# Optimization experiments

Measured on AMD Instinct MI355X. Metric: run time of the kernel, lower is better.

Reference implementation:

```python
import jax, jax.numpy as jnp
import numpy as np

WS = 8          # window size
NH = 4          # num heads
DIM = 64
HID = 256       # mlp_ratio * dim
EPS = 1e-5


def _rel_pos_index(ws):
    coords = np.stack(np.meshgrid(np.arange(ws), np.arange(ws), indexing='ij')).reshape(2, -1)
    rel = (coords[:, :, None] - coords[:, None, :]).transpose(1, 2, 0)  # (N,N,2)
    rel[..., 0] += ws - 1
    rel[..., 1] += ws - 1
    rel[..., 0] *= 2 * ws - 1
    return rel.sum(-1)  # (N,N)


def _layernorm(x, g, b):
    mu = x.mean(-1, keepdims=True)
    var = ((x - mu) ** 2).mean(-1, keepdims=True)
    return (x - mu) * jax.lax.rsqrt(var + EPS) * g + b


def setup_inputs() -> dict:
    key = jax.random.key(0)
    ks = jax.random.split(key, 16)
    s = 0.02
    return {
        'x': jax.random.normal(ks[0], (8, DIM, 256, 256), jnp.float32),
        'qkv_w': jax.random.normal(ks[1], (DIM, 3 * DIM), jnp.float32) * s,
        'qkv_b': jnp.zeros((3 * DIM,), jnp.float32),
        'proj_w': jax.random.normal(ks[2], (DIM, DIM), jnp.float32) * s,
        'proj_b': jnp.zeros((DIM,), jnp.float32),
        'rpb_table': jax.random.normal(ks[3], ((2 * WS - 1) ** 2, NH), jnp.float32) * s,
        'norm1_g': jnp.ones((DIM,), jnp.float32),
        'norm1_b': jnp.zeros((DIM,), jnp.float32),
        'norm2_g': jnp.ones((DIM,), jnp.float32),
        'norm2_b': jnp.zeros((DIM,), jnp.float32),
        'ffn_w1': jax.random.normal(ks[4], (DIM, HID), jnp.float32) * s,
        'ffn_b1': jnp.zeros((HID,), jnp.float32),
        'ffn_w2': jax.random.normal(ks[5], (HID, DIM), jnp.float32) * s,
        'ffn_w2_b': jnp.zeros((DIM,), jnp.float32),
        'dw_w': jax.random.normal(ks[6], (DIM, 1, 3, 3), jnp.float32) * s,
        'dw_b': jnp.zeros((DIM,), jnp.float32),
    }


def reference(x, qkv_w, qkv_b, proj_w, proj_b, rpb_table,
              norm1_g, norm1_b, norm2_g, norm2_b,
              ffn_w1, ffn_b1, ffn_w2, ffn_w2_b, dw_w, dw_b):
    B, C, H, W = x.shape
    ws, nh = WS, NH
    hd = C // nh
    N = ws * ws
    assert H % ws == 0 and W % ws == 0  # chosen shapes avoid reflect pad

    x_hw = jnp.transpose(x, (0, 2, 3, 1))  # (B,H,W,C)

    # --- window attention branch ---
    xn = _layernorm(x_hw, norm1_g, norm1_b)
    win = xn.reshape(B, H // ws, ws, W // ws, ws, C).transpose(0, 1, 3, 2, 4, 5)
    win = win.reshape(-1, N, C)  # (B*nW, N, C)

    qkv = win @ qkv_w + qkv_b  # (BnW, N, 3C)
    qkv = qkv.reshape(-1, N, 3, nh, hd).transpose(2, 0, 3, 1, 4)
    q, k, v = qkv[0], qkv[1], qkv[2]  # (BnW, nh, N, hd)

    scale = hd ** -0.5
    attn = jnp.einsum('bhnd,bhmd->bhnm', q, k) * scale
    idx = _rel_pos_index(ws)
    bias = rpb_table[idx.reshape(-1)].reshape(N, N, nh).transpose(2, 0, 1)  # (nh,N,N)
    attn = jax.nn.softmax(attn + bias[None], axis=-1)
    out = jnp.einsum('bhnm,bhmd->bhnd', attn, v)
    out = out.transpose(0, 2, 1, 3).reshape(-1, N, C)
    out = out @ proj_w + proj_b

    out = out.reshape(B, H // ws, W // ws, ws, ws, C).transpose(0, 1, 3, 2, 4, 5)
    out = out.reshape(B, H, W, C)
    x_hw = x_hw + out

    # --- FFN + depthwise conv branch ---
    xn = _layernorm(x_hw, norm2_g, norm2_b)
    ffn = jax.nn.gelu(xn @ ffn_w1 + ffn_b1, approximate=False) @ ffn_w2 + ffn_w2_b

    xc = jnp.transpose(x_hw, (0, 3, 1, 2))  # (B,C,H,W)
    xc = jax.lax.conv_general_dilated(
        xc, dw_w, window_strides=(1, 1), padding=((1, 1), (1, 1)),
        feature_group_count=C,
        dimension_numbers=('NCHW', 'OIHW', 'NCHW')) + dw_b[None, :, None, None]
    xc = jnp.transpose(xc, (0, 2, 3, 1))

    x_hw = x_hw + ffn + xc
    return jnp.transpose(x_hw, (0, 3, 1, 2))  # (B,C,H,W)
```

## Files before the change

kernel.cpp:

```cpp
#include <hip/hip_runtime.h>
#include <cmath>


typedef __attribute__((ext_vector_type(8))) short bf16x8;
typedef __attribute__((ext_vector_type(4))) short s16x4;
typedef __attribute__((ext_vector_type(4))) float f32x4;
typedef __attribute__((ext_vector_type(2))) __bf16 bfv2;
typedef __attribute__((ext_vector_type(4))) __bf16 bfv4;

static __device__ __forceinline__ unsigned short f2bf(float f) {
  return __builtin_bit_cast(unsigned short, (__bf16)f);
}
static __device__ __forceinline__ unsigned f2bf2(float a, float b) {
  bfv2 v; v.x = (__bf16)a; v.y = (__bf16)b;
  return __builtin_bit_cast(unsigned, v);
}
static __device__ __forceinline__ s16x4 f2bf4(f32x4 f) {
  bfv4 v; v.x = (__bf16)f[0]; v.y = (__bf16)f[1]; v.z = (__bf16)f[2]; v.w = (__bf16)f[3];
  return __builtin_bit_cast(s16x4, v);
}
static __device__ __forceinline__ float bf2f(unsigned short u) {
  union { unsigned u; float f; } v; v.u = ((unsigned)u) << 16;
  return v.f;
}
static __device__ __forceinline__ float bf2f_s(short s) { return bf2f((unsigned short)s); }

static __device__ __forceinline__ int swz(int row, int c) {
  return row * 72 + ((((c >> 3) ^ (row >> 3)) & 7) << 3) + (c & 7);
}
static __device__ __forceinline__ int swzg(int row, int g) {
  return row * 72 + (((g ^ (row >> 3)) & 7) << 3);
}

#define MFMA32(a, b, c) __builtin_amdgcn_mfma_f32_16x16x32_bf16(a, b, c, 0, 0, 0)

#if __has_builtin(__builtin_amdgcn_mfma_f32_16x16x16bf16_1k)
static __device__ __forceinline__ f32x4 MFMA16(s16x4 a, s16x4 b, f32x4 c) {
  return __builtin_amdgcn_mfma_f32_16x16x16bf16_1k(a, b, c, 0, 0, 0);
}
#else
static __device__ __forceinline__ f32x4 MFMA16(s16x4 a, s16x4 b, f32x4 c) {
  bf16x8 a8 = (bf16x8){a[0], a[1], a[2], a[3], 0, 0, 0, 0};
  bf16x8 b8 = (bf16x8){b[0], b[1], b[2], b[3], 0, 0, 0, 0};
  return __builtin_amdgcn_mfma_f32_16x16x32_bf16(a8, b8, c, 0, 0, 0);
}
#endif

__global__ void pack_weights_kernel(const float* __restrict__ qkv_w,
                                    const float* __restrict__ proj_w,
                                    const float* __restrict__ w1,
                                    const float* __restrict__ w2,
                                    const float* __restrict__ rpb,
                                    unsigned short* __restrict__ qkvt,
                                    unsigned short* __restrict__ projt,
                                    unsigned short* __restrict__ w1t,
                                    unsigned short* __restrict__ w2t,
                                    float* __restrict__ biasg) {
  const int t = blockIdx.x * 256 + threadIdx.x;
  {
    const int n = t >> 6, k = t & 63;
    if (n < 192) {
      float v = qkv_w[k * 192 + n];
      if (n < 64) v *= 0.25f;
      qkvt[t] = f2bf(v);
    }
    if (n < 64)  projt[t] = f2bf(proj_w[k * 64 + n]);
    w1t[t] = f2bf(w1[k * 256 + n]);
  }
  {
    const int n = t >> 8, k = t & 255;
    w2t[t] = f2bf(w2[k * 64 + n]);
  }
  {
    const int i = (t >> 6) & 63, j = t & 63, h = t >> 12;
    const int ridx = ((i >> 3) - (j >> 3) + 7) * 15 + ((i & 7) - (j & 7) + 7);
    biasg[t] = rpb[ridx * 4 + h];
  }
}

__global__ __launch_bounds__(512, 2)
void win_attn_kernel(const float* __restrict__ x,
                     const unsigned short* __restrict__ qkvt,
                     const float* __restrict__ qkv_b,
                     const unsigned short* __restrict__ projt,
                     const float* __restrict__ proj_b,
                     const float* __restrict__ biasg,
                     const float* __restrict__ n1g,
                     const float* __restrict__ n1b,
                     unsigned short* __restrict__ x1b)
{
  __shared__ unsigned short xw[2 * 4608];
  __shared__ unsigned short xn[2 * 4608];

  const int tid = threadIdx.x;
  const int bid = blockIdx.x;
  const int wid = ((bid & 7) << 9) | (bid >> 3);
  const int b   = wid >> 9;
  const int wy  = (wid >> 4) & 31;
  const int wxp = wid & 15;
  const int y0 = wy << 3, x0 = wxp << 4;

  const size_t imgbase = (size_t)b << 22;
#pragma unroll
  for (int i = 0; i < 16; ++i) {
    const int idx = i * 512 + tid;
    const int c = idx >> 7, t = idx & 127;
    const int ty = t >> 4, tx = t & 15;
    const float v = x[imgbase + ((size_t)c << 16) + (size_t)(y0 + ty) * 256 + (x0 + tx)];
    const int wn = tx >> 3, tok = (ty << 3) | (tx & 7);
    xw[wn * 4608 + swz(tok, c)] = f2bf(v);
  }
  __syncthreads();

  {
    const int t2 = tid >> 2, q = tid & 3;
    const int wn = t2 >> 6, tok = t2 & 63;
    const unsigned short* xwp = xw + wn * 4608;
    const bf16x8 h0 = *(const bf16x8*)&xwp[swzg(tok, 2 * q)];
    const bf16x8 h1 = *(const bf16x8*)&xwp[swzg(tok, 2 * q + 1)];
    float xv[16], s = 0.f, s2 = 0.f;
#pragma unroll
    for (int j = 0; j < 8; ++j) { xv[j] = bf2f_s(h0[j]); xv[8 + j] = bf2f_s(h1[j]); }
#pragma unroll
    for (int j = 0; j < 16; ++j) { s += xv[j]; s2 += xv[j] * xv[j]; }
    s  += __shfl_xor(s, 1);  s  += __shfl_xor(s, 2);
    s2 += __shfl_xor(s2, 1); s2 += __shfl_xor(s2, 2);
    const float mu   = s * 0.015625f;
    const float rstd = rsqrtf(s2 * 0.015625f - mu * mu + 1e-5f);
#pragma unroll
    for (int j = 0; j < 8; ++j) {
      const int c = q * 16 + j * 2;
      const float a0 = (xv[j * 2 + 0] - mu) * rstd * n1g[c]     + n1b[c];
      const float a1 = (xv[j * 2 + 1] - mu) * rstd * n1g[c + 1] + n1b[c + 1];
      *(unsigned*)&xn[wn * 4608 + swz(tok, c)] = f2bf2(a0, a1);
    }
  }
  __syncthreads();

  const int lane = tid & 63;
  const int w8   = tid >> 6;
  const int wn   = w8 >> 2;
  const int g    = w8 & 3;
  const int lr   = lane & 15;
  const int lg   = lane >> 4;
  const unsigned short* xnp = xn + wn * 4608;
  const unsigned short* xwp = xw + wn * 4608;
  unsigned short*       xnw = xn + wn * 4608;

  bf16x8 afr[4][2];
#pragma unroll
  for (int mt = 0; mt < 4; ++mt)
#pragma unroll
    for (int ks = 0; ks < 2; ++ks)
      afr[mt][ks] = *(const bf16x8*)&xnp[swzg(mt * 16 + lr, ks * 4 + lg)];
  __syncthreads();

  const int nbq = g * 16, nbk = 64 + g * 16, nbv = 128 + g * 16;
  f32x4 dqT[4], dkT[4], dv[4];
  {
    const float4 qb = *(const float4*)&qkv_b[nbq + lg * 4];
    const float4 kb = *(const float4*)&qkv_b[nbk + lg * 4];
    const float  vb = qkv_b[nbv + lr];
    const f32x4 qbv = (f32x4){qb.x * 0.25f, qb.y * 0.25f, qb.z * 0.25f, qb.w * 0.25f};
    const f32x4 kbv = (f32x4){kb.x, kb.y, kb.z, kb.w};
    const f32x4 vbv = (f32x4){vb, vb, vb, vb};
#pragma unroll
    for (int u = 0; u < 4; ++u) { dqT[u] = qbv; dkT[u] = kbv; dv[u] = vbv; }
  }
#pragma unroll
  for (int ks = 0; ks < 2; ++ks) {
    const bf16x8 wq = *(const bf16x8*)&qkvt[(nbq + lr) * 64 + ks * 32 + lg * 8];
    const bf16x8 wk = *(const bf16x8*)&qkvt[(nbk + lr) * 64 + ks * 32 + lg * 8];
    const bf16x8 wv = *(const bf16x8*)&qkvt[(nbv + lr) * 64 + ks * 32 + lg * 8];
#pragma unroll
    for (int u = 0; u < 4; ++u) {
      dqT[u] = MFMA32(wq, afr[u][ks], dqT[u]);
      dkT[u] = MFMA32(wk, afr[u][ks], dkT[u]);
      dv[u]  = MFMA32(afr[u][ks], wv, dv[u]);
    }
  }
  s16x4 qf[4], kf[4], vf[4];
#pragma unroll
  for (int u = 0; u < 4; ++u) { qf[u] = f2bf4(dqT[u]); kf[u] = f2bf4(dkT[u]); vf[u] = f2bf4(dv[u]); }

  f32x4 sacc[4][4];
#pragma unroll
  for (int mt = 0; mt < 4; ++mt)
#pragma unroll
    for (int nt = 0; nt < 4; ++nt) {
      const float4 bb = *(const float4*)&biasg[(g << 12) + (nt * 16 + lr) * 64 + mt * 16 + lg * 4];
      sacc[mt][nt] = MFMA16(kf[mt], qf[nt], (f32x4){bb.x, bb.y, bb.z, bb.w});
    }

  s16x4 pa[4][4];
#pragma unroll
  for (int nt = 0; nt < 4; ++nt) {
    float sum = 0.f;
#pragma unroll
    for (int mt = 0; mt < 4; ++mt)
#pragma unroll
      for (int r = 0; r < 4; ++r) { const float e = __expf(sacc[mt][nt][r]); sacc[mt][nt][r] = e; sum += e; }
    sum += __shfl_xor(sum, 16);
    sum += __shfl_xor(sum, 32);
    const float rs = 1.f / sum;
#pragma unroll
    for (int mt = 0; mt < 4; ++mt)
      pa[mt][nt] = f2bf4(sacc[mt][nt] * rs);
  }

  f32x4 o[4];
#pragma unroll
  for (int nt = 0; nt < 4; ++nt) {
    o[nt] = (f32x4){0,0,0,0};
#pragma unroll
    for (int mt = 0; mt < 4; ++mt)
      o[nt] = MFMA16(pa[mt][nt], vf[mt], o[nt]);
  }
#pragma unroll
  for (int nt = 0; nt < 4; ++nt)
#pragma unroll
    for (int r = 0; r < 4; ++r)
      xnw[swz(nt * 16 + lg * 4 + r, g * 16 + lr)] = f2bf(o[nt][r]);
  __syncthreads();

  {
    bf16x8 pa2[4][2];
#pragma unroll
    for (int mt = 0; mt < 4; ++mt)
#pragma unroll
      for (int ks = 0; ks < 2; ++ks)
        pa2[mt][ks] = *(const bf16x8*)&xnp[swzg(mt * 16 + lr, ks * 4 + lg)];
    __syncthreads();

    const float pbias = proj_b[g * 16 + lr];
    f32x4 d2[4];
#pragma unroll
    for (int mt = 0; mt < 4; ++mt) d2[mt] = (f32x4){pbias, pbias, pbias, pbias};
#pragma unroll
    for (int ks = 0; ks < 2; ++ks) {
      const bf16x8 pb = *(const bf16x8*)&projt[(g * 16 + lr) * 64 + ks * 32 + lg * 8];
#pragma unroll
      for (int mt = 0; mt < 4; ++mt)
        d2[mt] = MFMA32(pa2[mt][ks], pb, d2[mt]);
    }
#pragma unroll
    for (int mt = 0; mt < 4; ++mt)
#pragma unroll
      for (int r = 0; r < 4; ++r) {
        const int tok = mt * 16 + lg * 4 + r;
        const float val = d2[mt][r] + bf2f(xwp[swz(tok, g * 16 + lr)]);
        xnw[swz(tok, g * 16 + lr)] = f2bf(val);
      }
  }
  __syncthreads();

#pragma unroll
  for (int i = 0; i < 2; ++i) {
    const int u = i * 512 + tid;
    const int tk = u >> 3, gr = u & 7;
    const int wn2 = tk >> 6, tok = tk & 63;
    const bf16x8 v = *(const bf16x8*)&xn[wn2 * 4608 + swzg(tok, gr)];
    *(bf16x8*)&x1b[(((size_t)b * 256 + y0 + (tok >> 3)) * 256 + x0 + wn2 * 8 + (tok & 7)) * 64 + gr * 8] = v;
  }
}

__global__ __launch_bounds__(256, 2)
void ffn_conv_kernel(const unsigned short* __restrict__ x1b,
                     const float* __restrict__ n2g, const float* __restrict__ n2b,
                     const unsigned short* __restrict__ w1t, const float* __restrict__ b1,
                     const unsigned short* __restrict__ w2t, const float* __restrict__ b2,
                     const float* __restrict__ dww, const float* __restrict__ dwb,
                     float* __restrict__ out)
{
  __shared__ __align__(16) unsigned short pool[20000];
  unsigned short* x1h = pool;
  unsigned short* xnb = pool + 7200;
  unsigned short* hid = pool + 11808;
  float*          d2f = (float*)(pool + 7200);

  const int tid = threadIdx.x;
  const int bid = blockIdx.x;
  const int wid = ((bid & 7) << 10) | (bid >> 3);
  const int b  = wid >> 10;
  const int wy = (wid >> 5) & 31;
  const int wx = wid & 31;
  const int y0 = wy << 3, x0 = wx << 3;

  const int lane = tid & 63;
  const int g    = tid >> 6;
  const int lr   = lane & 15;
  const int lg   = lane >> 4;

#pragma unroll
  for (int i = 0; i < 7; ++i) {
    const int u = i * 256 + tid;
    if (u < 1600) {
      const int p = u >> 4, c4 = (u & 15) << 2;
      const int py = p / 10, px = p - py * 10;
      const int gy = y0 + py - 1, gx = x0 + px - 1;
      uint2 v = make_uint2(0u, 0u);
      if ((unsigned)gy < 256u && (unsigned)gx < 256u)
        v = *(const uint2*)&x1b[(((size_t)b * 256 + gy) * 256 + gx) * 64 + c4];
      *(uint2*)&x1h[p * 72 + c4] = v;
    }
  }
  __syncthreads();

  {
    const int t = tid >> 2, q = tid & 3;
    const int pp = ((t >> 3) + 1) * 10 + (t & 7) + 1;
    const bf16x8 h0 = *(const bf16x8*)&x1h[pp * 72 + q * 16];
    const bf16x8 h1 = *(const bf16x8*)&x1h[pp * 72 + q * 16 + 8];
    float xv[16], s = 0.f, s2 = 0.f;
#pragma unroll
    for (int j = 0; j < 8; ++j) { xv[j] = bf2f_s(h0[j]); xv[8 + j] = bf2f_s(h1[j]); }
#pragma unroll
    for (int j = 0; j < 16; ++j) { s += xv[j]; s2 += xv[j] * xv[j]; }
    s  += __shfl_xor(s, 1);  s  += __shfl_xor(s, 2);
    s2 += __shfl_xor(s2, 1); s2 += __shfl_xor(s2, 2);
    const float mu   = s * 0.015625f;
    const float rstd = rsqrtf(s2 * 0.015625f - mu * mu + 1e-5f);
#pragma unroll
    for (int j = 0; j < 8; ++j) {
      const int c = q * 16 + j * 2;
      const float a0 = (xv[j * 2 + 0] - mu) * rstd * n2g[c]     + n2b[c];
      const float a1 = (xv[j * 2 + 1] - mu) * rstd * n2g[c + 1] + n2b[c + 1];
      *(unsigned*)&xnb[swz(t, c)] = f2bf2(a0, a1);
    }
  }
  __syncthreads();

  bf16x8 afr[4][2];
#pragma unroll
  for (int mt = 0; mt < 4; ++mt)
#pragma unroll
    for (int ks = 0; ks < 2; ++ks)
      afr[mt][ks] = *(const bf16x8*)&xnb[swzg(mt * 16 + lr, ks * 4 + lg)];

  const float b2n = b2[g * 16 + lr];
  f32x4 d2[4];
#pragma unroll
  for (int mt = 0; mt < 4; ++mt) d2[mt] = (f32x4){b2n, b2n, b2n, b2n};

#pragma unroll
  for (int half = 0; half < 2; ++half) {
#pragma unroll
    for (int nt = 0; nt < 2; ++nt) {
      const int nb = half * 128 + g * 32 + nt * 16;
      const float4 bb = *(const float4*)&b1[nb + lg * 4];
      f32x4 d1[4];
#pragma unroll
      for (int mt = 0; mt < 4; ++mt) d1[mt] = (f32x4){bb.x, bb.y, bb.z, bb.w};
#pragma unroll
      for (int ks = 0; ks < 2; ++ks) {
        const bf16x8 aw = *(const bf16x8*)&w1t[(nb + lr) * 64 + ks * 32 + lg * 8];
#pragma unroll
        for (int mt = 0; mt < 4; ++mt)
          d1[mt] = MFMA32(aw, afr[mt][ks], d1[mt]);
      }
#pragma unroll
      for (int mt = 0; mt < 4; ++mt) {
        f32x4 hv;
#pragma unroll
        for (int r = 0; r < 4; ++r) {
          const float e = __expf(-1.702f * d1[mt][r]);
          hv[r] = __fdividef(d1[mt][r], 1.f + e);
        }
        const s16x4 pk = f2bf4(hv);
        const int row  = mt * 16 + lr;
        const int nl   = g * 32 + nt * 16 + lg * 4;
        const int addr = row * 128 + (((nl >> 3) ^ (row & 7)) << 3) + (nl & 7);
        *(s16x4*)&hid[addr] = pk;
      }
    }
    __syncthreads();

#pragma unroll
    for (int ks2 = 0; ks2 < 4; ++ks2) {
      const bf16x8 bw = *(const bf16x8*)&w2t[(g * 16 + lr) * 256 + half * 128 + ks2 * 32 + lg * 8];
#pragma unroll
      for (int mt = 0; mt < 4; ++mt) {
        const int row  = mt * 16 + lr;
        const int gran = ks2 * 4 + lg;
        const bf16x8 ah = *(const bf16x8*)&hid[row * 128 + ((gran ^ (row & 7)) << 3)];
        d2[mt] = MFMA32(ah, bw, d2[mt]);
      }
    }
    __syncthreads();
  }

  {
#pragma unroll
    for (int mt = 0; mt < 4; ++mt)
#pragma unroll
      for (int r = 0; r < 4; ++r)
        d2f[(mt * 16 + lg * 4 + r) * 65 + g * 16 + lr] = d2[mt][r];
  }
  __syncthreads();

  {
    const int cty = lane >> 3, ctx = lane & 7;
    float cacc[16];
#pragma unroll
    for (int i = 0; i < 16; ++i) cacc[i] = dwb[g * 16 + i];
#pragma unroll
    for (int dy = 0; dy < 3; ++dy)
#pragma unroll
      for (int dx = 0; dx < 3; ++dx) {
        const int p = (cty + dy) * 10 + (ctx + dx);
        const bf16x8 h0 = *(const bf16x8*)&x1h[p * 72 + g * 16];
        const bf16x8 h1 = *(const bf16x8*)&x1h[p * 72 + g * 16 + 8];
        const bool ctr = (dy == 1) && (dx == 1);
#pragma unroll
        for (int i = 0; i < 8; ++i) {
          float w0  = dww[(g * 16 + i) * 9     + dy * 3 + dx];
          float w1_ = dww[(g * 16 + 8 + i) * 9 + dy * 3 + dx];
          if (ctr) { w0 += 1.f; w1_ += 1.f; }
          cacc[i]     += w0  * bf2f_s(h0[i]);
          cacc[8 + i] += w1_ * bf2f_s(h1[i]);
        }
      }
    const size_t obase = ((size_t)b * 64 + g * 16) * 65536 + (size_t)(y0 + cty) * 256 + (x0 + ctx);
#pragma unroll
    for (int i = 0; i < 16; ++i)
      out[obase + (size_t)i * 65536] = cacc[i] + d2f[lane * 65 + g * 16 + i];
  }
}

extern "C" void kernel_launch(void* const* d_in, const int* in_sizes, int n_in,
                              void* d_out, int out_size, void* d_ws, size_t ws_size,
                              hipStream_t stream) {
  const float* x      = (const float*)d_in[0];
  const float* qkv_w  = (const float*)d_in[1];
  const float* qkv_b  = (const float*)d_in[2];
  const float* proj_w = (const float*)d_in[3];
  const float* proj_b = (const float*)d_in[4];
  const float* rpb    = (const float*)d_in[5];
  const float* n1g    = (const float*)d_in[6];
  const float* n1b    = (const float*)d_in[7];
  const float* n2g    = (const float*)d_in[8];
  const float* n2b    = (const float*)d_in[9];
  const float* w1     = (const float*)d_in[10];
  const float* b1     = (const float*)d_in[11];
  const float* w2     = (const float*)d_in[12];
  const float* b2     = (const float*)d_in[13];
  const float* dww    = (const float*)d_in[14];
  const float* dwb    = (const float*)d_in[15];
  float* out = (float*)d_out;

  unsigned short* x1bf = (unsigned short*)d_ws;
  unsigned short* wbuf = (unsigned short*)((char*)d_ws + 67108864);
  unsigned short* qkvt  = wbuf;
  unsigned short* projt = wbuf + 12288;
  unsigned short* w1t   = wbuf + 16384;
  unsigned short* w2t   = wbuf + 32768;
  float* biasg = (float*)((char*)d_ws + 67108864 + 98304);

  pack_weights_kernel<<<64, 256, 0, stream>>>(qkv_w, proj_w, w1, w2, rpb,
                                              qkvt, projt, w1t, w2t, biasg);
  win_attn_kernel<<<4096, 512, 0, stream>>>(x, qkvt, qkv_b, projt, proj_b,
                                            biasg, n1g, n1b, x1bf);
  ffn_conv_kernel<<<8192, 256, 0, stream>>>(x1bf, n2g, n2b, w1t, b1, w2t, b2,
                                            dww, dwb, out);
}
```

Before: 308.2 us.

## Vectorize window loads, reorder FFN kernel to shrink LDS, use exp2

The attention kernel now loads the NCHW input as float4, four pixels per thread, and scatters them into the swizzled LDS tile, instead of issuing one scalar load per element. The FFN/conv kernel now reads the LayerNorm input for its 8x8 tile straight from global memory and runs both FFN matmuls first. Only then does it load the 10x10 halo into LDS for the depthwise conv, so the buffers can share memory and the LDS pool drops from 20000 to 15520 shorts. The GELU-sigmoid exponent uses a hardware exp2 builtin with a folded constant. The aim is fewer load instructions, higher occupancy from the smaller LDS footprint, and cheaper transcendentals, at the cost of re-reading centre pixels from global memory.

Result: faster. 297.7 us (-3.4%).

```diff
diff --git a/kernel.cpp b/kernel.cpp
--- a/kernel.cpp
+++ b/kernel.cpp
@@ -24,6 +24,12 @@
   return v.f;
 }
 static __device__ __forceinline__ float bf2f_s(short s) { return bf2f((unsigned short)s); }
+
+#if __has_builtin(__builtin_amdgcn_exp2f)
+static __device__ __forceinline__ float fast_exp2(float x) { return __builtin_amdgcn_exp2f(x); }
+#else
+static __device__ __forceinline__ float fast_exp2(float x) { return __expf(x * 0.6931471805599453f); }
+#endif
 
 static __device__ __forceinline__ int swz(int row, int c) {
   return row * 72 + ((((c >> 3) ^ (row >> 3)) & 7) << 3) + (c & 7);
@@ -102,13 +108,19 @@
 
   const size_t imgbase = (size_t)b << 22;
 #pragma unroll
-  for (int i = 0; i < 16; ++i) {
-    const int idx = i * 512 + tid;
-    const int c = idx >> 7, t = idx & 127;
-    const int ty = t >> 4, tx = t & 15;
-    const float v = x[imgbase + ((size_t)c << 16) + (size_t)(y0 + ty) * 256 + (x0 + tx)];
-    const int wn = tx >> 3, tok = (ty << 3) | (tx & 7);
-    xw[wn * 4608 + swz(tok, c)] = f2bf(v);
+  for (int i = 0; i < 4; ++i) {
+    const int u = i * 512 + tid;
+    const int c = u >> 5;
+    const int rem = u & 31;
+    const int ty = rem >> 2, txq = rem & 3;
+    const float4 v = *(const float4*)&x[imgbase + ((size_t)c << 16) +
+                                        (size_t)(y0 + ty) * 256 + x0 + txq * 4];
+    unsigned short* dst = xw + (txq >> 1) * 4608;
+    const int tokb = (ty << 3) | ((txq & 1) << 2);
+    dst[swz(tokb + 0, c)] = f2bf(v.x);
+    dst[swz(tokb + 1, c)] = f2bf(v.y);
+    dst[swz(tokb + 2, c)] = f2bf(v.z);
+    dst[swz(tokb + 3, c)] = f2bf(v.w);
   }
   __syncthreads();
 
@@ -132,7 +144,7 @@
       const int c = q * 16 + j * 2;
       const float a0 = (xv[j * 2 + 0] - mu) * rstd * n1g[c]     + n1b[c];
       const float a1 = (xv[j * 2 + 1] - mu) * rstd * n1g[c + 1] + n1b[c + 1];
-      *(unsigned*)&xn[wn * 4608 + swz(tok, c)] = f2bf2(a0, a1);
+      *(unsigned*)&xn[wn * 4608 + swz(t2 & 63, c)] = f2bf2(a0, a1);
     }
   }
   __syncthreads();
@@ -272,10 +284,10 @@
                      const float* __restrict__ dww, const float* __restrict__ dwb,
                      float* __restrict__ out)
 {
-  __shared__ __align__(16) unsigned short pool[20000];
+  __shared__ __align__(16) unsigned short pool[15520];
+  unsigned short* xnb = pool;
+  unsigned short* hid = pool + 4608;
   unsigned short* x1h = pool;
-  unsigned short* xnb = pool + 7200;
-  unsigned short* hid = pool + 11808;
   float*          d2f = (float*)(pool + 7200);
 
   const int tid = threadIdx.x;
@@ -290,6 +302,89 @@
   const int g    = tid >> 6;
   const int lr   = lane & 15;
   const int lg   = lane >> 4;
+
+  {
+    const int t = tid >> 2, q = tid & 3;
+    const size_t tbase = (((size_t)b * 256 + y0 + (t >> 3)) * 256 + x0 + (t & 7)) * 64 + q * 16;
+    const bf16x8 h0 = *(const bf16x8*)&x1b[tbase];
+    const bf16x8 h1 = *(const bf16x8*)&x1b[tbase + 8];
+    float xv[16], s = 0.f, s2 = 0.f;
+#pragma unroll
+    for (int j = 0; j < 8; ++j) { xv[j] = bf2f_s(h0[j]); xv[8 + j] = bf2f_s(h1[j]); }
+#pragma unroll
+    for (int j = 0; j < 16; ++j) { s += xv[j]; s2 += xv[j] * xv[j]; }
+    s  += __shfl_xor(s, 1);  s  += __shfl_xor(s, 2);
+    s2 += __shfl_xor(s2, 1); s2 += __shfl_xor(s2, 2);
+    const float mu   = s * 0.015625f;
+    const float rstd = rsqrtf(s2 * 0.015625f - mu * mu + 1e-5f);
+#pragma unroll
+    for (int j = 0; j < 8; ++j) {
+      const int c = q * 16 + j * 2;
+      const float a0 = (xv[j * 2 + 0] - mu) * rstd * n2g[c]     + n2b[c];
+      const float a1 = (xv[j * 2 + 1] - mu) * rstd * n2g[c + 1] + n2b[c + 1];
+      *(unsigned*)&xnb[swz(t, c)] = f2bf2(a0, a1);
+    }
+  }
+  __syncthreads();
+
+  bf16x8 afr[4][2];
+#pragma unroll
+  for (int mt = 0; mt < 4; ++mt)
+#pragma unroll
+    for (int ks = 0; ks < 2; ++ks)
+      afr[mt][ks] = *(const bf16x8*)&xnb[swzg(mt * 16 + lr, ks * 4 + lg)];
+
+  const float b2n = b2[g * 16 + lr];
+  f32x4 d2[4];
+#pragma unroll
+  for (int mt = 0; mt < 4; ++mt) d2[mt] = (f32x4){b2n, b2n, b2n, b2n};
+
+#pragma unroll
+  for (int half = 0; half < 2; ++half) {
+#pragma unroll
+    for (int nt = 0; nt < 2; ++nt) {
+      const int nb = half * 128 + g * 32 + nt * 16;
+      const float4 bb = *(const float4*)&b1[nb + lg * 4];
+      f32x4 d1[4];
+#pragma unroll
+      for (int mt = 0; mt < 4; ++mt) d1[mt] = (f32x4){bb.x, bb.y, bb.z, bb.w};
+#pragma unroll
+      for (int ks = 0; ks < 2; ++ks) {
+        const bf16x8 aw = *(const bf16x8*)&w1t[(nb + lr) * 64 + ks * 32 + lg * 8];
+#pragma unroll
+        for (int mt = 0; mt < 4; ++mt)
+          d1[mt] = MFMA32(aw, afr[mt][ks], d1[mt]);
+      }
+#pragma unroll
+      for (int mt = 0; mt < 4; ++mt) {
+        f32x4 hv;
+#pragma unroll
+        for (int r = 0; r < 4; ++r) {
+          const float e = fast_exp2(d1[mt][r] * -2.4554669f);
+          hv[r] = __fdividef(d1[mt][r], 1.f + e);
+        }
+        const s16x4 pk = f2bf4(hv);
+        const int row  = mt * 16 + lr;
+        const int nl   = g * 32 + nt * 16 + lg * 4;
+        const int addr = row * 128 + (((nl >> 3) ^ (row & 7)) << 3) + (nl & 7);
+        *(s16x4*)&hid[addr] = pk;
+      }
+    }
+    __syncthreads();
+
+#pragma unroll
+    for (int ks2 = 0; ks2 < 4; ++ks2) {
+      const bf16x8 bw = *(const bf16x8*)&w2t[(g * 16 + lr) * 256 + half * 128 + ks2 * 32 + lg * 8];
+#pragma unroll
+      for (int mt = 0; mt < 4; ++mt) {
+        const int row  = mt * 16 + lr;
+        const int gran = ks2 * 4 + lg;
+        const bf16x8 ah = *(const bf16x8*)&hid[row * 128 + ((gran ^ (row & 7)) << 3)];
+        d2[mt] = MFMA32(ah, bw, d2[mt]);
+      }
+    }
+    __syncthreads();
+  }
 
 #pragma unroll
   for (int i = 0; i < 7; ++i) {
@@ -304,91 +399,6 @@
       *(uint2*)&x1h[p * 72 + c4] = v;
     }
   }
-  __syncthreads();
-
-  {
-    const int t = tid >> 2, q = tid & 3;
-    const int pp = ((t >> 3) + 1) * 10 + (t & 7) + 1;
-    const bf16x8 h0 = *(const bf16x8*)&x1h[pp * 72 + q * 16];
-    const bf16x8 h1 = *(const bf16x8*)&x1h[pp * 72 + q * 16 + 8];
-    float xv[16], s = 0.f, s2 = 0.f;
-#pragma unroll
-    for (int j = 0; j < 8; ++j) { xv[j] = bf2f_s(h0[j]); xv[8 + j] = bf2f_s(h1[j]); }
-#pragma unroll
-    for (int j = 0; j < 16; ++j) { s += xv[j]; s2 += xv[j] * xv[j]; }
-    s  += __shfl_xor(s, 1);  s  += __shfl_xor(s, 2);
-    s2 += __shfl_xor(s2, 1); s2 += __shfl_xor(s2, 2);
-    const float mu   = s * 0.015625f;
-    const float rstd = rsqrtf(s2 * 0.015625f - mu * mu + 1e-5f);
-#pragma unroll
-    for (int j = 0; j < 8; ++j) {
-      const int c = q * 16 + j * 2;
-      const float a0 = (xv[j * 2 + 0] - mu) * rstd * n2g[c]     + n2b[c];
-      const float a1 = (xv[j * 2 + 1] - mu) * rstd * n2g[c + 1] + n2b[c + 1];
-      *(unsigned*)&xnb[swz(t, c)] = f2bf2(a0, a1);
-    }
-  }
-  __syncthreads();
-
-  bf16x8 afr[4][2];
-#pragma unroll
-  for (int mt = 0; mt < 4; ++mt)
-#pragma unroll
-    for (int ks = 0; ks < 2; ++ks)
-      afr[mt][ks] = *(const bf16x8*)&xnb[swzg(mt * 16 + lr, ks * 4 + lg)];
-
-  const float b2n = b2[g * 16 + lr];
-  f32x4 d2[4];
-#pragma unroll
-  for (int mt = 0; mt < 4; ++mt) d2[mt] = (f32x4){b2n, b2n, b2n, b2n};
-
-#pragma unroll
-  for (int half = 0; half < 2; ++half) {
-#pragma unroll
-    for (int nt = 0; nt < 2; ++nt) {
-      const int nb = half * 128 + g * 32 + nt * 16;
-      const float4 bb = *(const float4*)&b1[nb + lg * 4];
-      f32x4 d1[4];
-#pragma unroll
-      for (int mt = 0; mt < 4; ++mt) d1[mt] = (f32x4){bb.x, bb.y, bb.z, bb.w};
-#pragma unroll
-      for (int ks = 0; ks < 2; ++ks) {
-        const bf16x8 aw = *(const bf16x8*)&w1t[(nb + lr) * 64 + ks * 32 + lg * 8];
-#pragma unroll
-        for (int mt = 0; mt < 4; ++mt)
-          d1[mt] = MFMA32(aw, afr[mt][ks], d1[mt]);
-      }
-#pragma unroll
-      for (int mt = 0; mt < 4; ++mt) {
-        f32x4 hv;
-#pragma unroll
-        for (int r = 0; r < 4; ++r) {
-          const float e = __expf(-1.702f * d1[mt][r]);
-          hv[r] = __fdividef(d1[mt][r], 1.f + e);
-        }
-        const s16x4 pk = f2bf4(hv);
-        const int row  = mt * 16 + lr;
-        const int nl   = g * 32 + nt * 16 + lg * 4;
-        const int addr = row * 128 + (((nl >> 3) ^ (row & 7)) << 3) + (nl & 7);
-        *(s16x4*)&hid[addr] = pk;
-      }
-    }
-    __syncthreads();
-
-#pragma unroll
-    for (int ks2 = 0; ks2 < 4; ++ks2) {
-      const bf16x8 bw = *(const bf16x8*)&w2t[(g * 16 + lr) * 256 + half * 128 + ks2 * 32 + lg * 8];
-#pragma unroll
-      for (int mt = 0; mt < 4; ++mt) {
-        const int row  = mt * 16 + lr;
-        const int gran = ks2 * 4 + lg;
-        const bf16x8 ah = *(const bf16x8*)&hid[row * 128 + ((gran ^ (row & 7)) << 3)];
-        d2[mt] = MFMA32(ah, bw, d2[mt]);
-      }
-    }
-    __syncthreads();
-  }
-
   {
 #pragma unroll
     for (int mt = 0; mt < 4; ++mt)
```
